# Kernel optimization log

Measured on AMD Instinct MI355X. Metric: run time of the kernel, lower is better.

The kernel has to match this reference:

```python
import jax, jax.numpy as jnp
import numpy as np

N_NODES = 50000
N_EDGES = 800000
N_GRAPHS = 64
F_IN, F_HID, F_OUT = 128, 128, 16


def _graph_conv(x, W, b, src, dst, activation=None):
    """DGL GraphConv with norm='both': D_out^{-1/2} A^T D_in^{-1/2} X W + b."""
    n = x.shape[0]
    ones = jnp.ones((src.shape[0],), dtype=x.dtype)
    deg_out = jnp.clip(jax.ops.segment_sum(ones, src, num_segments=n), 1.0)
    deg_in = jnp.clip(jax.ops.segment_sum(ones, dst, num_segments=n), 1.0)
    h = x * jax.lax.rsqrt(deg_out)[:, None]          # scale by src out-degree
    agg = jax.ops.segment_sum(h[src], dst, num_segments=n)  # gather+scatter-add
    agg = agg * jax.lax.rsqrt(deg_in)[:, None]       # scale by dst in-degree
    out = agg @ W + b
    if activation is not None:
        out = activation(out)
    return out


def setup_inputs() -> dict:
    key = jax.random.key(0)
    ks = jax.random.split(key, 6)
    x = jax.random.normal(ks[0], (N_NODES, F_IN), dtype=jnp.float32)
    W1 = jax.random.normal(ks[1], (F_IN, F_HID), dtype=jnp.float32) * (F_IN ** -0.5)
    b1 = jnp.zeros((F_HID,), dtype=jnp.float32)
    W2 = jax.random.normal(ks[2], (F_HID, F_OUT), dtype=jnp.float32) * (F_HID ** -0.5)
    b2 = jnp.zeros((F_OUT,), dtype=jnp.float32)
    src = jax.random.randint(ks[3], (N_EDGES,), 0, N_NODES, dtype=jnp.int32)
    dst = jax.random.randint(ks[4], (N_EDGES,), 0, N_NODES, dtype=jnp.int32)
    graph_ids = jnp.sort(jax.random.randint(ks[5], (N_NODES,), 0, N_GRAPHS, dtype=jnp.int32))
    return {"x": x, "W1": W1, "b1": b1, "W2": W2, "b2": b2,
            "src": src, "dst": dst, "graph_ids": graph_ids}


def reference(x, W1, b1, W2, b2, src, dst, graph_ids):
    h = _graph_conv(x, W1, b1, src, dst, activation=jax.nn.relu)
    h = _graph_conv(h, W2, b2, src, dst, activation=None)
    # dgl.mean_nodes: per-graph mean over nodes
    sums = jax.ops.segment_sum(h, graph_ids, num_segments=N_GRAPHS)
    counts = jnp.clip(jax.ops.segment_sum(jnp.ones((N_NODES,), h.dtype), graph_ids,
                                          num_segments=N_GRAPHS), 1.0)
    return sums / counts[:, None]
```

## Files before the change

### kernel.cpp

```cpp
#include <hip/hip_runtime.h>
#include <hip/hip_bf16.h>

#define N_NODES_C 50000
#define N_EDGES_C 800000
#define N_GRAPHS_C 64
#define NBKT 782
#define BKTP 784
#define CHUNK 4096
#define NBLK_E 196

typedef __attribute__((ext_vector_type(8))) short bf16x8;
typedef __attribute__((ext_vector_type(4))) float f32x4;

__device__ __forceinline__ unsigned short f2bf(float f) {
    unsigned u = __float_as_uint(f);
    unsigned r = (u + 0x7FFFu + ((u >> 16) & 1u)) >> 16;
    return (unsigned short)r;
}

__global__ __launch_bounds__(256) void k_hist(
    const int* __restrict__ src, const int* __restrict__ dst,
    int* __restrict__ hmatD, int* __restrict__ hmatS, int nE)
{
    __shared__ int hD[BKTP], hS[BKTP];
    const int tid = threadIdx.x, blk = blockIdx.x;
    for (int i = tid; i < BKTP; i += 256) { hD[i] = 0; hS[i] = 0; }
    __syncthreads();
    const int base = blk * CHUNK;
    for (int i = tid; i < CHUNK; i += 256) {
        int e = base + i;
        if (e < nE) {
            atomicAdd(&hD[dst[e] >> 6], 1);
            atomicAdd(&hS[src[e] >> 6], 1);
        }
    }
    __syncthreads();
    for (int i = tid; i < BKTP; i += 256) {
        hmatD[blk * BKTP + i] = hD[i];
        hmatS[blk * BKTP + i] = hS[i];
    }
}

__global__ __launch_bounds__(1024) void k_bscan(
    const int* __restrict__ hmatD, const int* __restrict__ hmatS,
    int* __restrict__ bbaseD, int* __restrict__ bbaseS,
    float* __restrict__ accbuf)
{
    __shared__ int part[1024];
    const int tid = threadIdx.x;
    const int* hm = blockIdx.x ? hmatS : hmatD;
    int* bb = blockIdx.x ? bbaseS : bbaseD;
    if (blockIdx.x == 0) accbuf[tid] = 0.f;
    int v = 0;
    if (tid < NBKT)
        for (int blk = 0; blk < NBLK_E; ++blk) v += hm[blk * BKTP + tid];
    part[tid] = v;
    __syncthreads();
    for (int off = 1; off < 1024; off <<= 1) {
        int t = (tid >= off) ? part[tid - off] : 0;
        __syncthreads();
        part[tid] += t;
        __syncthreads();
    }
    if (tid < NBKT) bb[tid] = part[tid] - v;
    if (tid == NBKT - 1) bb[NBKT] = part[tid];
}

__global__ __launch_bounds__(256) void k_boff(
    const int* __restrict__ hmatD, const int* __restrict__ hmatS,
    const int* __restrict__ bbaseD, const int* __restrict__ bbaseS,
    int* __restrict__ offmatD, int* __restrict__ offmatS,
    const float* __restrict__ W1, const float* __restrict__ W2,
    unsigned short* __restrict__ w1f, unsigned short* __restrict__ w2f)
{
    __shared__ int part[256];
    const int b = blockIdx.x, tid = threadIdx.x;
    const int* hm = blockIdx.y ? hmatS : hmatD;
    const int* bb = blockIdx.y ? bbaseS : bbaseD;
    int* om = blockIdx.y ? offmatS : offmatD;
    int v = (tid < NBLK_E) ? hm[tid * BKTP + b] : 0;
    part[tid] = v;
    __syncthreads();
    for (int off = 1; off < 256; off <<= 1) {
        int t = (tid >= off) ? part[tid - off] : 0;
        __syncthreads();
        part[tid] += t;
        __syncthreads();
    }
    if (tid < NBLK_E) om[tid * BKTP + b] = bb[b] + part[tid] - v;

    if (blockIdx.y == 1 && b < 9) {
        int t = b * 256 + tid;
        if (t < 2048) {
            int kk = t >> 9, nt = (t >> 6) & 7, l = t & 63;
            int kb = kk * 32 + ((l >> 4) << 3), n = nt * 16 + (l & 15);
            ushort4 lo, hi;
            lo.x = f2bf(W1[(kb + 0) * 128 + n]); lo.y = f2bf(W1[(kb + 1) * 128 + n]);
            lo.z = f2bf(W1[(kb + 2) * 128 + n]); lo.w = f2bf(W1[(kb + 3) * 128 + n]);
            hi.x = f2bf(W1[(kb + 4) * 128 + n]); hi.y = f2bf(W1[(kb + 5) * 128 + n]);
            hi.z = f2bf(W1[(kb + 6) * 128 + n]); hi.w = f2bf(W1[(kb + 7) * 128 + n]);
            ((ushort4*)(w1f + t * 8))[0] = lo;
            ((ushort4*)(w1f + t * 8))[1] = hi;
        } else if (t < 2304) {
            int t2 = t - 2048;
            int kk = t2 >> 6, l = t2 & 63;
            int kb = kk * 32 + ((l >> 4) << 3), n = l & 15;
            ushort4 lo, hi;
            lo.x = f2bf(W2[(kb + 0) * 16 + n]); lo.y = f2bf(W2[(kb + 1) * 16 + n]);
            lo.z = f2bf(W2[(kb + 2) * 16 + n]); lo.w = f2bf(W2[(kb + 3) * 16 + n]);
            hi.x = f2bf(W2[(kb + 4) * 16 + n]); hi.y = f2bf(W2[(kb + 5) * 16 + n]);
            hi.z = f2bf(W2[(kb + 6) * 16 + n]); hi.w = f2bf(W2[(kb + 7) * 16 + n]);
            ((ushort4*)(w2f + t2 * 8))[0] = lo;
            ((ushort4*)(w2f + t2 * 8))[1] = hi;
        }
    }
}

__global__ __launch_bounds__(256) void k_scat(
    const int* __restrict__ src, const int* __restrict__ dst,
    const int* __restrict__ offmatD, const int* __restrict__ offmatS,
    unsigned* __restrict__ ed, unsigned char* __restrict__ es, int nE)
{
    __shared__ int curD[BKTP], curS[BKTP];
    const int tid = threadIdx.x, blk = blockIdx.x;
    for (int i = tid; i < BKTP; i += 256) {
        curD[i] = offmatD[blk * BKTP + i];
        curS[i] = offmatS[blk * BKTP + i];
    }
    __syncthreads();
    const int base = blk * CHUNK;
    for (int i = tid; i < CHUNK; i += 256) {
        int e = base + i;
        if (e < nE) {
            unsigned s = (unsigned)src[e], d = (unsigned)dst[e];
            int pD = atomicAdd(&curD[d >> 6], 1);
            ed[pD] = (d << 16) | s;
            int pS = atomicAdd(&curS[s >> 6], 1);
            es[pS] = (unsigned char)(s & 63u);
        }
    }
}

__global__ __launch_bounds__(256) void k_bucket(
    const unsigned* __restrict__ ed, const unsigned char* __restrict__ es,
    const int* __restrict__ bbaseD, const int* __restrict__ bbaseS,
    const float* __restrict__ x,
    int* __restrict__ rowptr, float* __restrict__ rsI, float* __restrict__ rsO,
    unsigned short* __restrict__ csr_src, unsigned short* __restrict__ xs, int nV)
{
    __shared__ int cnt[64], cur[64];
    __shared__ float rs[64];
    const int tid = threadIdx.x;
    const int side = (blockIdx.x >= NBKT);
    const int b = side ? blockIdx.x - NBKT : blockIdx.x;

    if (tid < 64) cnt[tid] = 0;
    __syncthreads();

    if (!side) {
        const int lo = bbaseD[b], hi = bbaseD[b + 1];
        for (int j = lo + tid; j < hi; j += 256)
            atomicAdd(&cnt[(ed[j] >> 16) & 63u], 1);
        __syncthreads();
        if (tid < 64) {
            int c = cnt[tid];
            int v = c;
#pragma unroll
            for (int off = 1; off < 64; off <<= 1) {
                int n = __shfl_up(v, off, 64);
                if (tid >= off) v += n;
            }
            int excl = v - c;
            int node = b * 64 + tid;
            if (node <= nV) rowptr[node] = lo + excl;
            if (node < nV) rsI[node] = rsqrtf((float)max(c, 1));
            cur[tid] = excl;
        }
        __syncthreads();
        for (int j = lo + tid; j < hi; j += 256) {
            unsigned v = ed[j];
            int p = atomicAdd(&cur[(v >> 16) & 63u], 1);
            csr_src[lo + p] = (unsigned short)(v & 0xFFFFu);
        }
    } else {
        const int lo = bbaseS[b], hi = bbaseS[b + 1];
        for (int j = lo + tid; j < hi; j += 256)
            atomicAdd(&cnt[es[j]], 1);
        __syncthreads();
        if (tid < 64) {
            int node = b * 64 + tid;
            float r = rsqrtf((float)max(cnt[tid], 1));
            if (node < nV) rsO[node] = r;
            rs[tid] = r;
        }
        __syncthreads();
        for (int q = tid; q < 64 * 32; q += 256) {
            int n = q >> 5, c = q & 31;
            int node = b * 64 + n;
            if (node < nV) {
                float wgt = rs[n];
                float4 a = ((const float4*)(x + (size_t)node * 128))[c];
                ushort4 o;
                o.x = f2bf(a.x * wgt); o.y = f2bf(a.y * wgt);
                o.z = f2bf(a.z * wgt); o.w = f2bf(a.w * wgt);
                ((ushort4*)(xs + (size_t)node * 128))[c] = o;
            }
        }
    }
}

#define ACC8(vv)                                         \
    acc[0] += __uint_as_float((vv).x << 16);             \
    acc[1] += __uint_as_float((vv).x & 0xFFFF0000u);     \
    acc[2] += __uint_as_float((vv).y << 16);             \
    acc[3] += __uint_as_float((vv).y & 0xFFFF0000u);     \
    acc[4] += __uint_as_float((vv).z << 16);             \
    acc[5] += __uint_as_float((vv).z & 0xFFFF0000u);     \
    acc[6] += __uint_as_float((vv).w << 16);             \
    acc[7] += __uint_as_float((vv).w & 0xFFFF0000u);

__global__ __launch_bounds__(256) void k_agg1b(
    const unsigned short* __restrict__ xs, const int* __restrict__ rowptr,
    const unsigned short* __restrict__ csr_src, const float* __restrict__ rsI,
    unsigned short* __restrict__ agg1b, int nV)
{
    long long t = (long long)blockIdx.x * blockDim.x + threadIdx.x;
    int v = (int)(t >> 6);
    int lane = (int)(t & 63);
    if (v >= nV) return;
    int g = lane >> 4, fl = lane & 15;
    int beg = rowptr[v], end = rowptr[v + 1];
    float acc[8];
#pragma unroll
    for (int k = 0; k < 8; ++k) acc[k] = 0.f;

    int j = beg + g;
    while (j + 12 < end) {
        int s0 = csr_src[j], s1 = csr_src[j + 4], s2 = csr_src[j + 8], s3 = csr_src[j + 12];
        uint4 w0 = *(const uint4*)(xs + (size_t)s0 * 128 + fl * 8);
        uint4 w1 = *(const uint4*)(xs + (size_t)s1 * 128 + fl * 8);
        uint4 w2 = *(const uint4*)(xs + (size_t)s2 * 128 + fl * 8);
        uint4 w3 = *(const uint4*)(xs + (size_t)s3 * 128 + fl * 8);
        ACC8(w0); ACC8(w1); ACC8(w2); ACC8(w3);
        j += 16;
    }
    while (j + 4 < end) {
        int s0 = csr_src[j], s1 = csr_src[j + 4];
        uint4 w0 = *(const uint4*)(xs + (size_t)s0 * 128 + fl * 8);
        uint4 w1 = *(const uint4*)(xs + (size_t)s1 * 128 + fl * 8);
        ACC8(w0); ACC8(w1);
        j += 8;
    }
    if (j < end) {
        int s = csr_src[j];
        uint4 w0 = *(const uint4*)(xs + (size_t)s * 128 + fl * 8);
        ACC8(w0);
    }
#pragma unroll
    for (int k = 0; k < 8; ++k) {
        acc[k] += __shfl_xor(acc[k], 16, 64);
        acc[k] += __shfl_xor(acc[k], 32, 64);
    }
    float ri = rsI[v];
    if (g < 2) {
        ushort4 o;
        o.x = f2bf(acc[g * 4 + 0] * ri);
        o.y = f2bf(acc[g * 4 + 1] * ri);
        o.z = f2bf(acc[g * 4 + 2] * ri);
        o.w = f2bf(acc[g * 4 + 3] * ri);
        *(ushort4*)(agg1b + (size_t)v * 128 + fl * 8 + g * 4) = o;
    }
}

__global__ __launch_bounds__(256) void k_mfma(
    const unsigned short* __restrict__ agg1b, const float* __restrict__ b1,
    const unsigned short* __restrict__ w1f, const unsigned short* __restrict__ w2f,
    const float* __restrict__ rsO, unsigned short* __restrict__ y, int nV)
{
    __shared__ __align__(16) unsigned short h1[64 * 136];
    const int tid = threadIdx.x;
    const int w = tid >> 6, l = tid & 63;
    const int lr = l & 15, lg = l >> 4;
    const int row0 = blockIdx.x * 64;

    bf16x8 a[4];
    const unsigned short* abase = agg1b + (size_t)(row0 + w * 16 + lr) * 128 + lg * 8;
#pragma unroll
    for (int kk = 0; kk < 4; ++kk)
        a[kk] = *(const bf16x8*)(abase + kk * 32);

    f32x4 acc[8];
#pragma unroll
    for (int nt = 0; nt < 8; ++nt) acc[nt] = (f32x4){0.f, 0.f, 0.f, 0.f};

#pragma unroll
    for (int nt = 0; nt < 8; ++nt)
#pragma unroll
        for (int kk = 0; kk < 4; ++kk) {
            bf16x8 b = *(const bf16x8*)(w1f + ((kk * 8 + nt) * 64 + l) * 8);
            acc[nt] = __builtin_amdgcn_mfma_f32_16x16x32_bf16(a[kk], b, acc[nt], 0, 0, 0);
        }

#pragma unroll
    for (int nt = 0; nt < 8; ++nt) {
        float bb = b1[nt * 16 + lr];
#pragma unroll
        for (int i = 0; i < 4; ++i) {
            float h = fmaxf(acc[nt][i] + bb, 0.f);
            h1[(w * 16 + lg * 4 + i) * 136 + nt * 16 + lr] = f2bf(h);
        }
    }
    __syncthreads();

    f32x4 acc2 = (f32x4){0.f, 0.f, 0.f, 0.f};
#pragma unroll
    for (int kk = 0; kk < 4; ++kk) {
        bf16x8 a2 = *(const bf16x8*)(&h1[(w * 16 + lr) * 136 + kk * 32 + lg * 8]);
        bf16x8 b2 = *(const bf16x8*)(w2f + (kk * 64 + l) * 8);
        acc2 = __builtin_amdgcn_mfma_f32_16x16x32_bf16(a2, b2, acc2, 0, 0, 0);
    }
#pragma unroll
    for (int i = 0; i < 4; ++i) {
        int r = row0 + w * 16 + lg * 4 + i;
        if (r < nV) y[(size_t)r * 16 + lr] = f2bf(acc2[i] * rsO[r]);
    }
}

__global__ __launch_bounds__(256) void k_agg2p(
    const unsigned short* __restrict__ y, const int* __restrict__ rowptr,
    const unsigned short* __restrict__ csr_src, const float* __restrict__ rsI,
    const int* __restrict__ gid, float* __restrict__ accbuf, int nV)
{
    const int tid = threadIdx.x;
    const int lane = tid & 63, f = lane & 15, g4 = lane >> 4;
    const int wid = blockIdx.x * 4 + (tid >> 6);
    int v0 = wid * 8;
    if (v0 >= nV) return;
    int vend = min(v0 + 8, nV);
    float racc = 0.f;
    int curg = gid[v0];
    for (int v = v0; v < vend; ++v) {
        int beg = rowptr[v], end = rowptr[v + 1];
        float acc = 0.f;
        int j = beg + g4;
        while (j + 4 < end) {
            int s0 = csr_src[j], s1 = csr_src[j + 4];
            unsigned u0 = y[(size_t)s0 * 16 + f];
            unsigned u1 = y[(size_t)s1 * 16 + f];
            acc += __uint_as_float(u0 << 16) + __uint_as_float(u1 << 16);
            j += 8;
        }
        if (j < end) {
            unsigned u = y[(size_t)csr_src[j] * 16 + f];
            acc += __uint_as_float(u << 16);
        }
        acc += __shfl_xor(acc, 16, 64);
        acc += __shfl_xor(acc, 32, 64);
        int gg = gid[v];
        if (gg != curg) {
            if (g4 == 0 && racc != 0.f) unsafeAtomicAdd(&accbuf[curg * 16 + f], racc);
            racc = 0.f;
            curg = gg;
        }
        racc += acc * rsI[v];
    }
    if (g4 == 0 && racc != 0.f) unsafeAtomicAdd(&accbuf[curg * 16 + f], racc);
}

__device__ __forceinline__ int lowerb(const int* __restrict__ a, int n, int key) {
    int lo = 0, hi = n;
    while (lo < hi) { int m = (lo + hi) >> 1; if (a[m] < key) lo = m + 1; else hi = m; }
    return lo;
}

__global__ __launch_bounds__(256) void k_fin(
    const float* __restrict__ accbuf, const int* __restrict__ gid,
    const float* __restrict__ b2, float* __restrict__ out, int nV)
{
    int t = threadIdx.x;
    int g = t >> 2, f0 = (t & 3) * 4;
    int lo = lowerb(gid, nV, g);
    int hi = lowerb(gid, nV, g + 1);
    int n = hi - lo;
    float inv = (n > 0) ? 1.f / (float)n : 0.f;
#pragma unroll
    for (int k = 0; k < 4; ++k) {
        int f = f0 + k;
        out[g * 16 + f] = (n > 0) ? accbuf[g * 16 + f] * inv + b2[f] : 0.f;
    }
}

extern "C" void kernel_launch(void* const* d_in, const int* in_sizes, int n_in,
                              void* d_out, int out_size, void* d_ws, size_t ws_size,
                              hipStream_t stream) {
    const float* x   = (const float*)d_in[0];
    const float* W1  = (const float*)d_in[1];
    const float* b1  = (const float*)d_in[2];
    const float* W2  = (const float*)d_in[3];
    const float* b2  = (const float*)d_in[4];
    const int*   src = (const int*)d_in[5];
    const int*   dst = (const int*)d_in[6];
    const int*   gid = (const int*)d_in[7];
    float* out = (float*)d_out;

    int* p = (int*)d_ws;
    int*   bbaseD  = p;            p += 800;
    int*   bbaseS  = p;            p += 800;
    int*   rowptr  = p;            p += 50432;
    float* rsO     = (float*)p;    p += 50176;
    float* rsI     = (float*)p;    p += 50176;
    unsigned short* csr_src = (unsigned short*)p; p += 400128;
    unsigned short* w1f = (unsigned short*)p;     p += 8192;
    unsigned short* w2f = (unsigned short*)p;     p += 1024;
    unsigned short* y   = (unsigned short*)p;     p += 401408;
    float* accbuf  = (float*)p;    p += 1024;
    unsigned short* xs    = (unsigned short*)p;   p += 3211264;
    unsigned short* agg1b = (unsigned short*)p;   p += 3211264;
    int*   hmatD   = p;            p += 153664;
    int*   hmatS   = p;            p += 153664;
    int*   offmatD = p;            p += 153664;
    int*   offmatS = p;            p += 153664;
    unsigned*      ed = (unsigned*)p;      p += 800000;
    unsigned char* es = (unsigned char*)p; p += 200000;

    k_hist <<<NBLK_E, 256, 0, stream>>>(src, dst, hmatD, hmatS, N_EDGES_C);
    k_bscan<<<2, 1024, 0, stream>>>(hmatD, hmatS, bbaseD, bbaseS, accbuf);
    k_boff <<<dim3(NBKT, 2), 256, 0, stream>>>(hmatD, hmatS, bbaseD, bbaseS,
                                               offmatD, offmatS, W1, W2, w1f, w2f);
    k_scat <<<NBLK_E, 256, 0, stream>>>(src, dst, offmatD, offmatS, ed, es, N_EDGES_C);
    k_bucket<<<2 * NBKT, 256, 0, stream>>>(ed, es, bbaseD, bbaseS, x,
                                           rowptr, rsI, rsO, csr_src, xs, N_NODES_C);

    k_agg1b<<<(N_NODES_C * 64 + 255) / 256, 256, 0, stream>>>(xs, rowptr, csr_src, rsI, agg1b, N_NODES_C);
    k_mfma <<<(N_NODES_C + 63) / 64, 256, 0, stream>>>(agg1b, b1, w1f, w2f, rsO, y, N_NODES_C);
    k_agg2p<<<(N_NODES_C + 31) / 32, 256, 0, stream>>>(y, rowptr, csr_src, rsI, gid, accbuf, N_NODES_C);
    k_fin  <<<1, 256, 0, stream>>>(accbuf, gid, b2, out, N_NODES_C);
}
```

Baseline: 124.3 us.

## Fuse final mean into agg2 via last-block counter and widen gather to 2 features per lane

Removes the separate finalize kernel launch by having the last block of the layer-2 aggregation, found with a global atomic counter, compute the per-graph means. It also restructures the gather so each lane loads a 32-bit pair of bf16 features and processes 8 edges in parallel per node instead of 4. This saves a launch and halves the number of load instructions per edge. In exchange it adds a threadfence and an atomic per block, plus a longer shuffle reduction.

Measured after the change: 219.4 us. 1.77x slower.

```diff
diff --git a/kernel.cpp b/kernel.cpp
--- a/kernel.cpp
+++ b/kernel.cpp
@@ -44,13 +44,16 @@
 __global__ __launch_bounds__(1024) void k_bscan(
     const int* __restrict__ hmatD, const int* __restrict__ hmatS,
     int* __restrict__ bbaseD, int* __restrict__ bbaseS,
-    float* __restrict__ accbuf)
+    float* __restrict__ accbuf, int* __restrict__ fincnt)
 {
     __shared__ int part[1024];
     const int tid = threadIdx.x;
     const int* hm = blockIdx.x ? hmatS : hmatD;
     int* bb = blockIdx.x ? bbaseS : bbaseD;
-    if (blockIdx.x == 0) accbuf[tid] = 0.f;
+    if (blockIdx.x == 0) {
+        accbuf[tid] = 0.f;
+        if (tid == 0) *fincnt = 0;
+    }
     int v = 0;
     if (tid < NBKT)
         for (int blk = 0; blk < NBLK_E; ++blk) v += hm[blk * BKTP + tid];
@@ -326,67 +329,88 @@
     }
 }
 
-__global__ __launch_bounds__(256) void k_agg2p(
-    const unsigned short* __restrict__ y, const int* __restrict__ rowptr,
-    const unsigned short* __restrict__ csr_src, const float* __restrict__ rsI,
-    const int* __restrict__ gid, float* __restrict__ accbuf, int nV)
-{
-    const int tid = threadIdx.x;
-    const int lane = tid & 63, f = lane & 15, g4 = lane >> 4;
-    const int wid = blockIdx.x * 4 + (tid >> 6);
-    int v0 = wid * 8;
-    if (v0 >= nV) return;
-    int vend = min(v0 + 8, nV);
-    float racc = 0.f;
-    int curg = gid[v0];
-    for (int v = v0; v < vend; ++v) {
-        int beg = rowptr[v], end = rowptr[v + 1];
-        float acc = 0.f;
-        int j = beg + g4;
-        while (j + 4 < end) {
-            int s0 = csr_src[j], s1 = csr_src[j + 4];
-            unsigned u0 = y[(size_t)s0 * 16 + f];
-            unsigned u1 = y[(size_t)s1 * 16 + f];
-            acc += __uint_as_float(u0 << 16) + __uint_as_float(u1 << 16);
-            j += 8;
-        }
-        if (j < end) {
-            unsigned u = y[(size_t)csr_src[j] * 16 + f];
-            acc += __uint_as_float(u << 16);
-        }
-        acc += __shfl_xor(acc, 16, 64);
-        acc += __shfl_xor(acc, 32, 64);
-        int gg = gid[v];
-        if (gg != curg) {
-            if (g4 == 0 && racc != 0.f) unsafeAtomicAdd(&accbuf[curg * 16 + f], racc);
-            racc = 0.f;
-            curg = gg;
-        }
-        racc += acc * rsI[v];
-    }
-    if (g4 == 0 && racc != 0.f) unsafeAtomicAdd(&accbuf[curg * 16 + f], racc);
-}
-
 __device__ __forceinline__ int lowerb(const int* __restrict__ a, int n, int key) {
     int lo = 0, hi = n;
     while (lo < hi) { int m = (lo + hi) >> 1; if (a[m] < key) lo = m + 1; else hi = m; }
     return lo;
 }
 
-__global__ __launch_bounds__(256) void k_fin(
-    const float* __restrict__ accbuf, const int* __restrict__ gid,
-    const float* __restrict__ b2, float* __restrict__ out, int nV)
-{
-    int t = threadIdx.x;
-    int g = t >> 2, f0 = (t & 3) * 4;
-    int lo = lowerb(gid, nV, g);
-    int hi = lowerb(gid, nV, g + 1);
-    int n = hi - lo;
-    float inv = (n > 0) ? 1.f / (float)n : 0.f;
-#pragma unroll
-    for (int k = 0; k < 4; ++k) {
-        int f = f0 + k;
-        out[g * 16 + f] = (n > 0) ? accbuf[g * 16 + f] * inv + b2[f] : 0.f;
+__global__ __launch_bounds__(256) void k_agg2p(
+    const unsigned short* __restrict__ y, const int* __restrict__ rowptr,
+    const unsigned short* __restrict__ csr_src, const float* __restrict__ rsI,
+    const int* __restrict__ gid, float* __restrict__ accbuf,
+    int* __restrict__ fincnt, const float* __restrict__ b2,
+    float* __restrict__ out, int nV)
+{
+    __shared__ int lastFlag;
+    const int tid = threadIdx.x;
+    const int lane = tid & 63, fl8 = lane & 7, g8 = lane >> 3;
+    const int wid = blockIdx.x * 4 + (tid >> 6);
+    int v0 = wid * 8;
+    if (v0 < nV) {
+        int vend = min(v0 + 8, nV);
+        float rlo = 0.f, rhi = 0.f;
+        int curg = gid[v0];
+        for (int v = v0; v < vend; ++v) {
+            int beg = rowptr[v], end = rowptr[v + 1];
+            float alo = 0.f, ahi = 0.f;
+            int j = beg + g8;
+            while (j + 8 < end) {
+                int s0 = csr_src[j], s1 = csr_src[j + 8];
+                unsigned u0 = *(const unsigned*)(y + (size_t)s0 * 16 + fl8 * 2);
+                unsigned u1 = *(const unsigned*)(y + (size_t)s1 * 16 + fl8 * 2);
+                alo += __uint_as_float(u0 << 16) + __uint_as_float(u1 << 16);
+                ahi += __uint_as_float(u0 & 0xFFFF0000u) + __uint_as_float(u1 & 0xFFFF0000u);
+                j += 16;
+            }
+            if (j < end) {
+                unsigned u = *(const unsigned*)(y + (size_t)csr_src[j] * 16 + fl8 * 2);
+                alo += __uint_as_float(u << 16);
+                ahi += __uint_as_float(u & 0xFFFF0000u);
+            }
+#pragma unroll
+            for (int off = 8; off < 64; off <<= 1) {
+                alo += __shfl_xor(alo, off, 64);
+                ahi += __shfl_xor(ahi, off, 64);
+            }
+            int gg = gid[v];
+            if (gg != curg) {
+                if (g8 == 0) {
+                    if (rlo != 0.f) unsafeAtomicAdd(&accbuf[curg * 16 + fl8 * 2], rlo);
+                    if (rhi != 0.f) unsafeAtomicAdd(&accbuf[curg * 16 + fl8 * 2 + 1], rhi);
+                }
+                rlo = 0.f; rhi = 0.f;
+                curg = gg;
+            }
+            float ri = rsI[v];
+            rlo += alo * ri;
+            rhi += ahi * ri;
+        }
+        if (g8 == 0) {
+            if (rlo != 0.f) unsafeAtomicAdd(&accbuf[curg * 16 + fl8 * 2], rlo);
+            if (rhi != 0.f) unsafeAtomicAdd(&accbuf[curg * 16 + fl8 * 2 + 1], rhi);
+        }
+    }
+
+    __threadfence();
+    if (tid == 0) {
+        int prev = atomicAdd(fincnt, 1);
+        lastFlag = (prev == (int)gridDim.x - 1) ? 1 : 0;
+    }
+    __syncthreads();
+    if (lastFlag) {
+        __threadfence();
+        int g = tid >> 2, f0 = (tid & 3) * 4;
+        int lo = lowerb(gid, nV, g);
+        int hi = lowerb(gid, nV, g + 1);
+        int n = hi - lo;
+        float inv = (n > 0) ? 1.f / (float)n : 0.f;
+#pragma unroll
+        for (int k = 0; k < 4; ++k) {
+            int f = f0 + k;
+            float s = atomicAdd(&accbuf[g * 16 + f], 0.f);
+            out[g * 16 + f] = (n > 0) ? s * inv + b2[f] : 0.f;
+        }
     }
 }
 
@@ -414,6 +438,7 @@
     unsigned short* w2f = (unsigned short*)p;     p += 1024;
     unsigned short* y   = (unsigned short*)p;     p += 401408;
     float* accbuf  = (float*)p;    p += 1024;
+    int*   fincnt  = p;            p += 16;
     unsigned short* xs    = (unsigned short*)p;   p += 3211264;
     unsigned short* agg1b = (unsigned short*)p;   p += 3211264;
     int*   hmatD   = p;            p += 153664;
@@ -424,7 +449,7 @@
     unsigned char* es = (unsigned char*)p; p += 200000;
 
     k_hist <<<NBLK_E, 256, 0, stream>>>(src, dst, hmatD, hmatS, N_EDGES_C);
-    k_bscan<<<2, 1024, 0, stream>>>(hmatD, hmatS, bbaseD, bbaseS, accbuf);
+    k_bscan<<<2, 1024, 0, stream>>>(hmatD, hmatS, bbaseD, bbaseS, accbuf, fincnt);
     k_boff <<<dim3(NBKT, 2), 256, 0, stream>>>(hmatD, hmatS, bbaseD, bbaseS,
                                                offmatD, offmatS, W1, W2, w1f, w2f);
     k_scat <<<NBLK_E, 256, 0, stream>>>(src, dst, offmatD, offmatS, ed, es, N_EDGES_C);
@@ -433,6 +458,6 @@
 
     k_agg1b<<<(N_NODES_C * 64 + 255) / 256, 256, 0, stream>>>(xs, rowptr, csr_src, rsI, agg1b, N_NODES_C);
     k_mfma <<<(N_NODES_C + 63) / 64, 256, 0, stream>>>(agg1b, b1, w1f, w2f, rsO, y, N_NODES_C);
-    k_agg2p<<<(N_NODES_C + 31) / 32, 256, 0, stream>>>(y, rowptr, csr_src, rsI, gid, accbuf, N_NODES_C);
-    k_fin  <<<1, 256, 0, stream>>>(accbuf, gid, b2, out, N_NODES_C);
-}
+    k_agg2p<<<(N_NODES_C + 31) / 32, 256, 0, stream>>>(y, rowptr, csr_src, rsI, gid,
+                                                       accbuf, fincnt, b2, out, N_NODES_C);
+}
```
